# Optimization experiments

Hardware: AMD Instinct MI355X
Metric: run time of the kernel (lower is better)

Reference implementation:

```python
import jax, jax.numpy as jnp
import numpy as np

E = 16777216       # total edges across the batch
NG = 1024          # num_graphs
K = 32             # action_topk
TEMP = 1.0         # policy_temperature


def setup_inputs() -> dict:
    key = jax.random.key(0)
    k1, k2, k3, k4, k5 = jax.random.split(key, 5)
    edge_logits = jax.random.normal(k1, (E,), dtype=jnp.float32)
    edge_scores = jax.random.normal(k2, (E,), dtype=jnp.float32)
    stop_logits = jax.random.normal(k3, (NG,), dtype=jnp.float32)
    edge_batch = jnp.sort(jax.random.randint(k4, (E,), 0, NG)).astype(jnp.int64)
    candidate_mask = jax.random.randint(k5, (E,), 0, 2).astype(bool)
    return {
        'edge_logits': edge_logits,
        'edge_scores': edge_scores,
        'stop_logits': stop_logits,
        'edge_batch': edge_batch,
        'candidate_mask': candidate_mask,
    }


def _topk_edge_mask(edge_scores, edge_batch, candidate_mask):
    """Faithful port of _select_topk_candidate_edges, returning a boolean keep
    mask over all E edges (fixed shape; indices of kept edges are implicit)."""
    neg_inf = jnp.finfo(jnp.float32).min
    # Non-candidates get a sentinel segment NG and -inf score so they sort last.
    seg_key = jnp.where(candidate_mask, edge_batch, NG)
    score = jnp.where(candidate_mask, edge_scores.astype(jnp.float32), neg_inf)
    # Sort by score descending, then stable-sort by segment id
    order_score = jnp.argsort(-score)
    seg_by_score = seg_key[order_score]
    order_seg = jnp.argsort(seg_by_score)          # jax argsort is stable
    cand_sorted = order_score[order_seg]           # original edge ids, sorted
    seg_sorted = seg_by_score[order_seg]
    # rank within each segment = position - segment start (exclusive cumsum)
    counts = jnp.bincount(seg_sorted, length=NG + 1)
    start = jnp.concatenate([jnp.zeros((1,), counts.dtype), jnp.cumsum(counts)[:-1]])
    rank = jnp.arange(E) - start[seg_sorted]
    keep_sorted = (rank < K) & (seg_sorted < NG)
    return jnp.zeros((E,), dtype=bool).at[cand_sorted].set(keep_sorted)


def _segment_logsumexp_1d(logits, segment_ids, num_segments):
    """Faithful port of torch _segment_logsumexp_1d."""
    neg_inf = jnp.finfo(logits.dtype).min
    eps = jnp.finfo(logits.dtype).eps
    max_per = jnp.full((num_segments,), neg_inf, dtype=logits.dtype).at[segment_ids].max(logits)
    exp = jnp.exp(logits - max_per[segment_ids])
    sum_per = jnp.zeros((num_segments,), dtype=logits.dtype).at[segment_ids].add(exp)
    return jnp.log(jnp.maximum(sum_per, eps)) + max_per


def reference(edge_logits, edge_scores, stop_logits, edge_batch, candidate_mask):
    neg_inf = jnp.finfo(jnp.float32).min
    # Per-graph top-k pruning of candidate edges by edge_scores
    valid = _topk_edge_mask(edge_scores, edge_batch, candidate_mask)
    # Segmented temperature softmax over (valid edges + stop action)
    logits_t = edge_logits / TEMP
    stop_t = stop_logits / TEMP
    masked = jnp.where(valid, logits_t, neg_inf)
    lse_edges = _segment_logsumexp_1d(masked, edge_batch, NG)       # [NG]
    log_denom = jnp.logaddexp(lse_edges, stop_t)                    # [NG]
    log_prob_edge = jnp.where(valid, logits_t - log_denom[edge_batch], neg_inf)
    return log_prob_edge
```

## Files before the change

kernel.cpp:

```cpp
#include <hip/hip_runtime.h>
#include <float.h>

#define TPB 512
#define KTOP 32
#define BIN_CAP 1024

#define SENT_U32 0xFF7F0000u
#define VCLAMP 3.0e38f

__device__ __forceinline__ unsigned int f2u(float f){
  unsigned int u = __float_as_uint(f);
  return (u & 0x80000000u) ? ~u : (u | 0x80000000u);
}

__device__ int suffix_total(int* hist, int NB, int* gsum, int tid){
  int GS = NB >> 8;
  if (tid < 256){
    int p = 0, base = tid * GS;
    for (int j = 0; j < GS; ++j) p += hist[base + j];
    gsum[tid] = p;
  }
  __syncthreads();
  for (int d = 1; d < 256; d <<= 1){
    int v = 0;
    if (tid < 256 && tid + d < 256) v = gsum[tid + d];
    __syncthreads();
    if (tid < 256) gsum[tid] += v;
    __syncthreads();
  }
  return gsum[0];
}

__device__ int find_bin(int* hist, int NB, int* gsum, int R, int* s2, int tid,
                        int* above_out){
  int GS = NB >> 8;
  if (tid < 256){
    int St  = gsum[tid];
    int St1 = (tid < 255) ? gsum[tid + 1] : 0;
    if (R > St1 && R <= St) s2[0] = tid;
  }
  __syncthreads();
  if (tid == 0){
    int G = s2[0];
    int above = (G < 255) ? gsum[G + 1] : 0;
    int b = (G + 1) * GS - 1;
    for (; b > G * GS; --b){
      int h = hist[b];
      if (above + h >= R) break;
      above += h;
    }
    s2[0] = b; s2[1] = above;
  }
  __syncthreads();
  int bin = s2[0];
  *above_out = s2[1];
  __syncthreads();
  return bin;
}

__global__ void __launch_bounds__(TPB, 4)
fused_kernel(const float* __restrict__ logits,
             const float* __restrict__ scores,
             const float* __restrict__ stop_logits,
             const int* __restrict__ batch,
             const int* __restrict__ cmask,
             float* __restrict__ out, int E, int NG)
{
  __shared__ int hist[4096];
  __shared__ int gsum[256];
  __shared__ int s2[2];
  __shared__ int sbounds[2];
  __shared__ unsigned int bin_u[BIN_CAP];
  __shared__ int bin_i[BIN_CAP];
  __shared__ int ab_i[KTOP];
  __shared__ int vidx[KTOP];
  __shared__ float vlog[KTOP];
  __shared__ int cnt_bin, cnt_ab, vcnt;
  __shared__ float sh_logden;

  int tid = threadIdx.x;
  int g = blockIdx.x;

  if (tid < 2){
    int target = g + tid;
    int lo = 0, hi = E;
    while (lo < hi){
      int mid = (lo + hi) >> 1;
      if (batch[mid] < target) lo = mid + 1; else hi = mid;
    }
    sbounds[tid] = lo;
  }
  __syncthreads();
  int s = sbounds[0], e = sbounds[1];
  int s4 = (s + 3) & ~3; if (s4 > e) s4 = e;
  int e4 = e & ~3;       if (e4 < s4) e4 = s4;
  const int4*   cm4 = (const int4*)cmask;
  const float4* sc4 = (const float4*)scores;

  auto scan = [&](auto&& fn){
    int i = s + tid;  if (i < s4) fn(cmask[i], scores[i], i);
    int j = e4 + tid; if (j < e)  fn(cmask[j], scores[j], j);
    for (int q = (s4 >> 2) + tid, qe = (e4 >> 2); q < qe; q += TPB){
      int4 m = cm4[q]; float4 sc = sc4[q];
      int base = q << 2;
      fn(m.x, sc.x, base);     fn(m.y, sc.y, base + 1);
      fn(m.z, sc.z, base + 2); fn(m.w, sc.w, base + 3);
    }
  };

  for (int b = tid; b < 4096; b += TPB) hist[b] = 0;
  __syncthreads();
  scan([&](int m, float sc, int){ if (m) atomicAdd(&hist[f2u(sc) >> 20], 1); });
  __syncthreads();

  int T = suffix_total(hist, 4096, gsum, tid);
  bool sel = (T > KTOP);
  unsigned int prefix = 0; int pshift = 32; int R = KTOP;
  if (sel){
    int above;
    int b1 = find_bin(hist, 4096, gsum, R, s2, tid, &above);
    R -= above; prefix = (unsigned)b1; pshift = 20;
    int hcnt = hist[b1];
    __syncthreads();
    if (hcnt > BIN_CAP){
      for (int b = tid; b < 4096; b += TPB) hist[b] = 0;
      __syncthreads();
      scan([&](int m, float sc, int){
        if (m){ unsigned u = f2u(sc);
          if ((u >> 20) == prefix) atomicAdd(&hist[(u >> 8) & 0xFFFu], 1); }
      });
      __syncthreads();
      suffix_total(hist, 4096, gsum, tid);
      int b2 = find_bin(hist, 4096, gsum, R, s2, tid, &above);
      R -= above; prefix = (prefix << 12) | (unsigned)b2; pshift = 8;
      hcnt = hist[b2];
      __syncthreads();
      if (hcnt > BIN_CAP){
        for (int b = tid; b < 256; b += TPB) hist[b] = 0;
        __syncthreads();
        scan([&](int m, float sc, int){
          if (m){ unsigned u = f2u(sc);
            if ((u >> 8) == prefix) atomicAdd(&hist[u & 0xFFu], 1); }
        });
        __syncthreads();
        suffix_total(hist, 256, gsum, tid);
        int b3 = find_bin(hist, 256, gsum, R, s2, tid, &above);
        R -= above; prefix = (prefix << 8) | (unsigned)b3; pshift = 0;
        __syncthreads();
      }
    }
  }

  if (tid == 0){ cnt_bin = 0; cnt_ab = 0; vcnt = 0; }
  __syncthreads();
  if (sel){
    scan([&](int m, float sc, int idx){
      if (m){
        unsigned u = f2u(sc);
        unsigned hp = u >> pshift;
        if (hp == prefix){
          int sl = atomicAdd(&cnt_bin, 1);
          if (sl < BIN_CAP){ bin_u[sl] = u; bin_i[sl] = idx; }
        } else if (hp > prefix){
          int sl = atomicAdd(&cnt_ab, 1);
          if (sl < KTOP) ab_i[sl] = idx;
        }
      }
    });
  } else {
    scan([&](int m, float, int idx){
      if (m){
        int sl = atomicAdd(&vcnt, 1);
        if (sl < KTOP) vidx[sl] = idx;
      }
    });
  }
  __syncthreads();

  if (sel){
    int bn = min(cnt_bin, BIN_CAP);
    for (int jj = tid; jj < bn; jj += TPB){
      unsigned long long kj = ((unsigned long long)bin_u[jj] << 32)
                            | (unsigned long long)(unsigned)(~(unsigned)bin_i[jj]);
      int rank = 0;
      for (int k = 0; k < bn; ++k){
        unsigned long long kk2 = ((unsigned long long)bin_u[k] << 32)
                               | (unsigned long long)(unsigned)(~(unsigned)bin_i[k]);
        rank += (kk2 > kj) ? 1 : 0;
      }
      if (rank < R){
        int sl = atomicAdd(&vcnt, 1);
        if (sl < KTOP) vidx[sl] = bin_i[jj];
      }
    }
    int na = min(cnt_ab, KTOP);
    for (int jj = tid; jj < na; jj += TPB){
      int sl = atomicAdd(&vcnt, 1);
      if (sl < KTOP) vidx[sl] = ab_i[jj];
    }
    __syncthreads();
  }

  int c = min(vcnt, KTOP);
  if (tid < c) vlog[tid] = logits[vidx[tid]];
  __syncthreads();
  if (tid == 0){
    float stop = stop_logits[g];
    float logden;
    if (c == 0){
      logden = stop;
    } else {
      float m = -FLT_MAX;
      for (int j2 = 0; j2 < c; ++j2) m = fmaxf(m, vlog[j2]);
      float sum = 0.f;
      for (int j2 = 0; j2 < c; ++j2) sum += expf(vlog[j2] - m);
      float lse = logf(fmaxf(sum, FLT_EPSILON)) + m;
      float mx = fmaxf(lse, stop);
      float dd = fabsf(lse - stop);
      logden = mx + log1pf(expf(-dd));
    }
    sh_logden = logden;
  }

  const float SENT = __uint_as_float(SENT_U32);
  {
    int i = s + tid;  if (i < s4) out[i] = SENT;
    int j = e4 + tid; if (j < e)  out[j] = SENT;
    float4 sv = make_float4(SENT, SENT, SENT, SENT);
    for (int q = (s4 >> 2) + tid, qe = (e4 >> 2); q < qe; q += TPB)
      ((float4*)out)[q] = sv;
  }
  __syncthreads();

  if (tid < c){
    float val = vlog[tid] - sh_logden;
    if (!(val >= -VCLAMP)) val = -VCLAMP;
    if (val > VCLAMP)      val =  VCLAMP;
    out[vidx[tid]] = val;
  }
}

extern "C" void kernel_launch(void* const* d_in, const int* in_sizes, int n_in,
                              void* d_out, int out_size, void* d_ws, size_t ws_size,
                              hipStream_t stream){
  const float* edge_logits = (const float*)d_in[0];
  const float* edge_scores = (const float*)d_in[1];
  const float* stop_logits = (const float*)d_in[2];
  const int*   edge_batch  = (const int*)d_in[3];
  const int*   cmask       = (const int*)d_in[4];
  int E  = in_sizes[0];
  int NG = in_sizes[2];
  float* out = (float*)d_out;
  (void)d_ws; (void)ws_size;

  hipLaunchKernelGGL(fused_kernel, dim3(NG), dim3(TPB), 0, stream,
                     edge_logits, edge_scores, stop_logits, edge_batch, cmask,
                     out, E, NG);
}
```

Before: 264.3 us.

## Cache candidate mask as shared bitmap and fuse sentinel fill into first pass

The first scan now records the candidate mask as a per-graph shared-memory bitmap and writes the sentinel output in the same pass. Later scans read only scores and test candidacy from the bitmap, which avoids re-reading the int mask from global memory. The separate output-fill pass is removed. Block size drops to 256 threads with 8 blocks per CU, and histograms shrink to 11/11/10-bit radix digits to cut shared memory. The bitmap covers 32K edges per graph and falls back to global mask reads beyond that; the smaller bin capacity may trigger more refinement passes.

After: 263.7 us. About the same (-0.2%).

```diff
diff --git a/kernel.cpp b/kernel.cpp
--- a/kernel.cpp
+++ b/kernel.cpp
@@ -1,9 +1,10 @@
 #include <hip/hip_runtime.h>
 #include <float.h>
 
-#define TPB 512
+#define TPB 256
 #define KTOP 32
-#define BIN_CAP 1024
+#define BIN_CAP 512
+#define BMAP_WORDS 1024
 
 #define SENT_U32 0xFF7F0000u
 #define VCLAMP 3.0e38f
@@ -15,17 +16,14 @@
 
 __device__ int suffix_total(int* hist, int NB, int* gsum, int tid){
   int GS = NB >> 8;
-  if (tid < 256){
-    int p = 0, base = tid * GS;
-    for (int j = 0; j < GS; ++j) p += hist[base + j];
-    gsum[tid] = p;
-  }
+  int p = 0, base = tid * GS;
+  for (int j = 0; j < GS; ++j) p += hist[base + j];
+  gsum[tid] = p;
   __syncthreads();
   for (int d = 1; d < 256; d <<= 1){
-    int v = 0;
-    if (tid < 256 && tid + d < 256) v = gsum[tid + d];
-    __syncthreads();
-    if (tid < 256) gsum[tid] += v;
+    int v = (tid + d < 256) ? gsum[tid + d] : 0;
+    __syncthreads();
+    gsum[tid] += v;
     __syncthreads();
   }
   return gsum[0];
@@ -34,11 +32,9 @@
 __device__ int find_bin(int* hist, int NB, int* gsum, int R, int* s2, int tid,
                         int* above_out){
   int GS = NB >> 8;
-  if (tid < 256){
-    int St  = gsum[tid];
-    int St1 = (tid < 255) ? gsum[tid + 1] : 0;
-    if (R > St1 && R <= St) s2[0] = tid;
-  }
+  int St  = gsum[tid];
+  int St1 = (tid < 255) ? gsum[tid + 1] : 0;
+  if (R > St1 && R <= St) s2[0] = tid;
   __syncthreads();
   if (tid == 0){
     int G = s2[0];
@@ -58,7 +54,7 @@
   return bin;
 }
 
-__global__ void __launch_bounds__(TPB, 4)
+__global__ void __launch_bounds__(TPB, 8)
 fused_kernel(const float* __restrict__ logits,
              const float* __restrict__ scores,
              const float* __restrict__ stop_logits,
@@ -66,10 +62,11 @@
              const int* __restrict__ cmask,
              float* __restrict__ out, int E, int NG)
 {
-  __shared__ int hist[4096];
+  __shared__ int hist[2048];
   __shared__ int gsum[256];
   __shared__ int s2[2];
   __shared__ int sbounds[2];
+  __shared__ unsigned int bmap[BMAP_WORDS];
   __shared__ unsigned int bin_u[BIN_CAP];
   __shared__ int bin_i[BIN_CAP];
   __shared__ int ab_i[KTOP];
@@ -97,87 +94,108 @@
   const int4*   cm4 = (const int4*)cmask;
   const float4* sc4 = (const float4*)scores;
 
-  auto scan = [&](auto&& fn){
-    int i = s + tid;  if (i < s4) fn(cmask[i], scores[i], i);
-    int j = e4 + tid; if (j < e)  fn(cmask[j], scores[j], j);
+  for (int b = tid; b < 2048; b += TPB) hist[b] = 0;
+  for (int w = tid; w < BMAP_WORDS; w += TPB) bmap[w] = 0;
+  if (tid == 0){ cnt_bin = 0; cnt_ab = 0; vcnt = 0; }
+  __syncthreads();
+
+  const float SENT = __uint_as_float(SENT_U32);
+
+  auto p1 = [&](int m, float sc, int idx){
+    if (m){
+      unsigned u = f2u(sc);
+      atomicAdd(&hist[u >> 21], 1);
+      int rel = idx - s;
+      if (rel < BMAP_WORDS * 32) atomicOr(&bmap[rel >> 5], 1u << (rel & 31));
+    }
+  };
+  {
+    int i = s + tid;  if (i < s4){ p1(cmask[i], scores[i], i); out[i] = SENT; }
+    int j = e4 + tid; if (j < e) { p1(cmask[j], scores[j], j); out[j] = SENT; }
+    float4 sv = make_float4(SENT, SENT, SENT, SENT);
     for (int q = (s4 >> 2) + tid, qe = (e4 >> 2); q < qe; q += TPB){
       int4 m = cm4[q]; float4 sc = sc4[q];
       int base = q << 2;
-      fn(m.x, sc.x, base);     fn(m.y, sc.y, base + 1);
-      fn(m.z, sc.z, base + 2); fn(m.w, sc.w, base + 3);
-    }
+      p1(m.x, sc.x, base);     p1(m.y, sc.y, base + 1);
+      p1(m.z, sc.z, base + 2); p1(m.w, sc.w, base + 3);
+      ((float4*)out)[q] = sv;
+    }
+  }
+  __syncthreads();
+
+  auto is_cand = [&](int idx) -> bool {
+    int rel = idx - s;
+    if (rel < BMAP_WORDS * 32) return (bmap[rel >> 5] >> (rel & 31)) & 1u;
+    return cmask[idx] != 0;
   };
-
-  for (int b = tid; b < 4096; b += TPB) hist[b] = 0;
-  __syncthreads();
-  scan([&](int m, float sc, int){ if (m) atomicAdd(&hist[f2u(sc) >> 20], 1); });
-  __syncthreads();
-
-  int T = suffix_total(hist, 4096, gsum, tid);
+  auto scan_sc = [&](auto&& fn){
+    int i = s + tid;  if (i < s4) fn(scores[i], i);
+    int j = e4 + tid; if (j < e)  fn(scores[j], j);
+    for (int q = (s4 >> 2) + tid, qe = (e4 >> 2); q < qe; q += TPB){
+      float4 sc = sc4[q];
+      int base = q << 2;
+      fn(sc.x, base);     fn(sc.y, base + 1);
+      fn(sc.z, base + 2); fn(sc.w, base + 3);
+    }
+  };
+
+  int T = suffix_total(hist, 2048, gsum, tid);
   bool sel = (T > KTOP);
   unsigned int prefix = 0; int pshift = 32; int R = KTOP;
   if (sel){
     int above;
-    int b1 = find_bin(hist, 4096, gsum, R, s2, tid, &above);
-    R -= above; prefix = (unsigned)b1; pshift = 20;
+    int b1 = find_bin(hist, 2048, gsum, R, s2, tid, &above);
+    R -= above; prefix = (unsigned)b1; pshift = 21;
     int hcnt = hist[b1];
     __syncthreads();
     if (hcnt > BIN_CAP){
-      for (int b = tid; b < 4096; b += TPB) hist[b] = 0;
+      for (int b = tid; b < 2048; b += TPB) hist[b] = 0;
       __syncthreads();
-      scan([&](int m, float sc, int){
-        if (m){ unsigned u = f2u(sc);
-          if ((u >> 20) == prefix) atomicAdd(&hist[(u >> 8) & 0xFFFu], 1); }
+      scan_sc([&](float sc, int idx){
+        unsigned u = f2u(sc);
+        if ((u >> 21) == prefix && is_cand(idx))
+          atomicAdd(&hist[(u >> 10) & 0x7FFu], 1);
       });
       __syncthreads();
-      suffix_total(hist, 4096, gsum, tid);
-      int b2 = find_bin(hist, 4096, gsum, R, s2, tid, &above);
-      R -= above; prefix = (prefix << 12) | (unsigned)b2; pshift = 8;
+      suffix_total(hist, 2048, gsum, tid);
+      int b2 = find_bin(hist, 2048, gsum, R, s2, tid, &above);
+      R -= above; prefix = (prefix << 11) | (unsigned)b2; pshift = 10;
       hcnt = hist[b2];
       __syncthreads();
       if (hcnt > BIN_CAP){
-        for (int b = tid; b < 256; b += TPB) hist[b] = 0;
+        for (int b = tid; b < 1024; b += TPB) hist[b] = 0;
         __syncthreads();
-        scan([&](int m, float sc, int){
-          if (m){ unsigned u = f2u(sc);
-            if ((u >> 8) == prefix) atomicAdd(&hist[u & 0xFFu], 1); }
+        scan_sc([&](float sc, int idx){
+          unsigned u = f2u(sc);
+          if ((u >> 10) == prefix && is_cand(idx))
+            atomicAdd(&hist[u & 0x3FFu], 1);
         });
         __syncthreads();
-        suffix_total(hist, 256, gsum, tid);
-        int b3 = find_bin(hist, 256, gsum, R, s2, tid, &above);
-        R -= above; prefix = (prefix << 8) | (unsigned)b3; pshift = 0;
+        suffix_total(hist, 1024, gsum, tid);
+        int b3 = find_bin(hist, 1024, gsum, R, s2, tid, &above);
+        R -= above; prefix = (prefix << 10) | (unsigned)b3; pshift = 0;
         __syncthreads();
       }
     }
   }
 
-  if (tid == 0){ cnt_bin = 0; cnt_ab = 0; vcnt = 0; }
-  __syncthreads();
   if (sel){
-    scan([&](int m, float sc, int idx){
-      if (m){
-        unsigned u = f2u(sc);
-        unsigned hp = u >> pshift;
-        if (hp == prefix){
-          int sl = atomicAdd(&cnt_bin, 1);
-          if (sl < BIN_CAP){ bin_u[sl] = u; bin_i[sl] = idx; }
-        } else if (hp > prefix){
-          int sl = atomicAdd(&cnt_ab, 1);
-          if (sl < KTOP) ab_i[sl] = idx;
+    scan_sc([&](float sc, int idx){
+      unsigned u = f2u(sc);
+      unsigned hp = (pshift < 32) ? (u >> pshift) : 0u;
+      if (hp >= prefix){
+        if (is_cand(idx)){
+          if (hp == prefix){
+            int sl = atomicAdd(&cnt_bin, 1);
+            if (sl < BIN_CAP){ bin_u[sl] = u; bin_i[sl] = idx; }
+          } else {
+            int sl = atomicAdd(&cnt_ab, 1);
+            if (sl < KTOP) ab_i[sl] = idx;
+          }
         }
       }
     });
-  } else {
-    scan([&](int m, float, int idx){
-      if (m){
-        int sl = atomicAdd(&vcnt, 1);
-        if (sl < KTOP) vidx[sl] = idx;
-      }
-    });
-  }
-  __syncthreads();
-
-  if (sel){
+    __syncthreads();
     int bn = min(cnt_bin, BIN_CAP);
     for (int jj = tid; jj < bn; jj += TPB){
       unsigned long long kj = ((unsigned long long)bin_u[jj] << 32)
@@ -198,8 +216,26 @@
       int sl = atomicAdd(&vcnt, 1);
       if (sl < KTOP) vidx[sl] = ab_i[jj];
     }
-    __syncthreads();
-  }
+  } else {
+    int n = e - s;
+    int nw = (n + 31) >> 5; if (nw > BMAP_WORDS) nw = BMAP_WORDS;
+    for (int w = tid; w < nw; w += TPB){
+      unsigned bits = bmap[w];
+      while (bits){
+        int b = __ffs((int)bits) - 1;
+        bits &= bits - 1;
+        int sl = atomicAdd(&vcnt, 1);
+        if (sl < KTOP) vidx[sl] = s + (w << 5) + b;
+      }
+    }
+    for (int i = s + BMAP_WORDS * 32 + tid; i < e; i += TPB){
+      if (cmask[i]){
+        int sl = atomicAdd(&vcnt, 1);
+        if (sl < KTOP) vidx[sl] = i;
+      }
+    }
+  }
+  __syncthreads();
 
   int c = min(vcnt, KTOP);
   if (tid < c) vlog[tid] = logits[vidx[tid]];
@@ -221,15 +257,6 @@
     }
     sh_logden = logden;
   }
-
-  const float SENT = __uint_as_float(SENT_U32);
-  {
-    int i = s + tid;  if (i < s4) out[i] = SENT;
-    int j = e4 + tid; if (j < e)  out[j] = SENT;
-    float4 sv = make_float4(SENT, SENT, SENT, SENT);
-    for (int q = (s4 >> 2) + tid, qe = (e4 >> 2); q < qe; q += TPB)
-      ((float4*)out)[q] = sv;
-  }
   __syncthreads();
 
   if (tid < c){
```
